# Kernel tuning notes

Measured on AMD Instinct MI355X. Metric: run time of the kernel, lower is better.

The kernel has to match this reference:

```python
import jax, jax.numpy as jnp
import numpy as np

ATOM_DIM = 64
BOND_DIM = 64
B, N_ATOMS, N_BONDS = 32, 256, 512


def setup_inputs() -> dict:
    key = jax.random.key(0)
    k1, k2, k3, k4 = jax.random.split(key, 4)
    atom_state = jax.random.normal(k1, (B, N_ATOMS, ATOM_DIM), dtype=jnp.float32)
    bond_state = jax.random.normal(k2, (B, N_BONDS, BOND_DIM), dtype=jnp.float32)
    connectivity = jax.random.randint(k3, (B, N_BONDS, 2), 0, N_ATOMS, dtype=jnp.int64)
    # glorot-ish scale for the learned bond->matrix projection
    scale = (2.0 / (BOND_DIM + ATOM_DIM * ATOM_DIM)) ** 0.5
    bond_transform = jax.random.normal(k4, (BOND_DIM, ATOM_DIM * ATOM_DIM), dtype=jnp.float32) * scale
    return {
        "atom_state": atom_state,
        "bond_state": bond_state,
        "connectivity": connectivity,
        "bond_transform": bond_transform,
    }


def reference(atom_state, bond_state, connectivity, bond_transform):
    # src atom per edge: gather along atom axis with batch dim (tf.gather batch_dims=1)
    src_idx = connectivity[:, :, 0]                                  # [B, E]
    src_atoms = jnp.take_along_axis(
        atom_state, src_idx[:, :, None], axis=1)                    # [B, E, D]
    # bond embedding -> per-edge DxD matrix
    W = bond_transform.reshape(BOND_DIM, ATOM_DIM, ATOM_DIM)         # [K, D, D]
    bond_weights = jnp.einsum('bek,kij->beij', bond_state, W)        # [B, E, D, D]
    # per-edge matrix-vector message: A_e @ h_src
    messages = jnp.einsum('beij,bej->bei', bond_weights, src_atoms)  # [B, E, D]
    return messages
```

## Files before the change

### kernel.cpp

```cpp
#include <hip/hip_runtime.h>
#include <stdint.h>


#define NATOMS 256
#define DIM 64
#define BM 64

typedef _Float16 f16;
typedef _Float16 f16x2 __attribute__((ext_vector_type(2)));
typedef _Float16 f16x8 __attribute__((ext_vector_type(8)));
typedef float f32x16 __attribute__((ext_vector_type(16)));

#define AS1 __attribute__((address_space(1)))
#define AS3 __attribute__((address_space(3)))

union H8 { f16x8 v8; f16x2 v2[4]; };

static __device__ __forceinline__ void gll16(const void* g, void* l) {
    __builtin_amdgcn_global_load_lds((AS1 void*)(uintptr_t)g, (AS3 void*)l, 16, 0, 0);
}

__global__ __launch_bounds__(256) void prep_w2f(const float* __restrict__ bt,
                                                f16* __restrict__ w2f) {
    const int d  = blockIdx.x * 256 + threadIdx.x;
    const int kg = d >> 9, c = d & 511;
    const int wcq = c >> 8, s = (c >> 6) & 3, l = c & 63;
    const int i = (l & 31) + 32 * wcq;
    const int u = 2 * s + (l >> 5);
    const float* src = bt + (size_t)kg * 4096 + i * 64 + u * 8;
    const float4 p = *reinterpret_cast<const float4*>(src);
    const float4 q = *reinterpret_cast<const float4*>(src + 4);
    const f16x8 h = { (f16)p.x, (f16)p.y, (f16)p.z, (f16)p.w,
                      (f16)q.x, (f16)q.y, (f16)q.z, (f16)q.w };
    reinterpret_cast<f16x8*>(w2f)[d] = h;
}

__global__ __launch_bounds__(256, 1) void bond_msg(
    const float* __restrict__ atom, const float* __restrict__ bond,
    const int* __restrict__ conn, const f16* __restrict__ w2f,
    float* __restrict__ out)
{
    __shared__ __align__(16) unsigned char smem[32768];

    const int tid  = threadIdx.x;
    const int lane = tid & 63;
    const int w    = tid >> 6;
    const int wc   = w & 1;
    const int kh   = w >> 1;
    const int lo   = lane & 31;
    const int hi   = lane >> 5;
    const int blk  = blockIdx.x;
    const int bond0 = blk * BM;

    const int m0 = lo, m1 = lo + 32;
    const int ia0 = conn[(bond0 + m0) * 2];
    const int ia1 = conn[(bond0 + m1) * 2];
    const float* ar0 = atom + (size_t)(blk >> 3) * (NATOMS * DIM) + (size_t)ia0 * DIM;
    const float* ar1 = atom + (size_t)(blk >> 3) * (NATOMS * DIM) + (size_t)ia1 * DIM;
    f16x2 srcv[2][4][4];
    #pragma unroll
    for (int s = 0; s < 4; ++s) {
        const int j0 = s * 16 + hi * 8;
        float4 p0 = *reinterpret_cast<const float4*>(ar0 + j0);
        float4 p1 = *reinterpret_cast<const float4*>(ar0 + j0 + 4);
        float4 q0 = *reinterpret_cast<const float4*>(ar1 + j0);
        float4 q1 = *reinterpret_cast<const float4*>(ar1 + j0 + 4);
        srcv[0][s][0] = (f16x2){ (f16)p0.x, (f16)p0.y };
        srcv[0][s][1] = (f16x2){ (f16)p0.z, (f16)p0.w };
        srcv[0][s][2] = (f16x2){ (f16)p1.x, (f16)p1.y };
        srcv[0][s][3] = (f16x2){ (f16)p1.z, (f16)p1.w };
        srcv[1][s][0] = (f16x2){ (f16)q0.x, (f16)q0.y };
        srcv[1][s][1] = (f16x2){ (f16)q0.z, (f16)q0.w };
        srcv[1][s][2] = (f16x2){ (f16)q1.x, (f16)q1.y };
        srcv[1][s][3] = (f16x2){ (f16)q1.z, (f16)q1.w };
    }

    {
        const char* gb = reinterpret_cast<const char*>(bond + (size_t)bond0 * DIM);
        #pragma unroll
        for (int c = 0; c < 4; ++c)
            gll16(gb + w * 4096 + c * 1024 + lane * 16, smem + w * 4096 + c * 1024);
    }
    __syncthreads();

    {
        const float* bl = reinterpret_cast<const float*>(smem);
        unsigned* btw = reinterpret_cast<unsigned*>(smem + 16384);
        const int k = lane;
        #pragma unroll
        for (int mm = 0; mm < 16; ++mm) {
            const int m = w * 16 + mm;
            const f16 hh = (f16)bl[m * 64 + k];
            const f16x2 d = { hh, hh };
            btw[k * 64 + (m ^ (k & 31))] = __builtin_bit_cast(unsigned, d);
        }
    }
    __syncthreads();

    f32x16 acc0 = {};
    f32x16 acc1 = {};
    const unsigned* btl = reinterpret_cast<const unsigned*>(smem + 16384);
    const char* gw = reinterpret_cast<const char*>(w2f)
                   + (size_t)kh * 32 * 8192 + wc * 4096 + lane * 16;

    f16x8 bufA[4], bufB[4];
    #define LOADIT(buf, it) do {                                          \
        const char* _p = gw + (it) * 8192;                                \
        buf[0] = *reinterpret_cast<const f16x8*>(_p);                     \
        buf[1] = *reinterpret_cast<const f16x8*>(_p + 1024);              \
        buf[2] = *reinterpret_cast<const f16x8*>(_p + 2048);              \
        buf[3] = *reinterpret_cast<const f16x8*>(_p + 3072);              \
    } while (0)

    #define COMPIT(buf, it) do {                                          \
        const int _kg = kh * 32 + (it);                                   \
        const f16x2 _b0 = __builtin_bit_cast(f16x2,                       \
            btl[_kg * 64 + (m0 ^ (_kg & 31))]);                           \
        const f16x2 _b1 = __builtin_bit_cast(f16x2,                       \
            btl[_kg * 64 + (m1 ^ (_kg & 31))]);                           \
        _Pragma("unroll")                                                 \
        for (int s = 0; s < 4; ++s) {                                     \
            H8 _a0, _a1;                                                  \
            _Pragma("unroll")                                             \
            for (int t = 0; t < 4; ++t) {                                 \
                _a0.v2[t] = _b0 * srcv[0][s][t];                          \
                _a1.v2[t] = _b1 * srcv[1][s][t];                          \
            }                                                             \
            acc0 = __builtin_amdgcn_mfma_f32_32x32x16_f16(_a0.v8, buf[s], acc0, 0, 0, 0); \
            acc1 = __builtin_amdgcn_mfma_f32_32x32x16_f16(_a1.v8, buf[s], acc1, 0, 0, 0); \
        }                                                                 \
    } while (0)

    LOADIT(bufA, 0);
    for (int it = 0; it < 32; it += 2) {
        LOADIT(bufB, it + 1);
        COMPIT(bufA, it);
        if (it + 2 < 32) LOADIT(bufA, it + 2);
        COMPIT(bufB, it + 1);
    }

    if (kh == 1) {
        #pragma unroll
        for (int g = 0; g < 4; ++g) {
            float4 v0 = { acc0[4*g+0], acc0[4*g+1], acc0[4*g+2], acc0[4*g+3] };
            *reinterpret_cast<float4*>(smem + wc*8192 + g*1024 + lane*16) = v0;
            float4 v1 = { acc1[4*g+0], acc1[4*g+1], acc1[4*g+2], acc1[4*g+3] };
            *reinterpret_cast<float4*>(smem + wc*8192 + (g+4)*1024 + lane*16) = v1;
        }
    }
    __syncthreads();
    if (kh == 0) {
        #pragma unroll
        for (int g = 0; g < 4; ++g) {
            float4 v0 = *reinterpret_cast<const float4*>(smem + wc*8192 + g*1024 + lane*16);
            acc0[4*g+0] += v0.x; acc0[4*g+1] += v0.y; acc0[4*g+2] += v0.z; acc0[4*g+3] += v0.w;
            float4 v1 = *reinterpret_cast<const float4*>(smem + wc*8192 + (g+4)*1024 + lane*16);
            acc1[4*g+0] += v1.x; acc1[4*g+1] += v1.y; acc1[4*g+2] += v1.z; acc1[4*g+3] += v1.w;
        }
        const int colb = 32 * wc + lo;
        #pragma unroll
        for (int r = 0; r < 16; ++r) {
            const int rl = (r & 3) + 8 * (r >> 2) + 4 * hi;
            out[(size_t)(bond0 + rl) * 64 + colb]      = acc0[r];
            out[(size_t)(bond0 + 32 + rl) * 64 + colb] = acc1[r];
        }
    }
}

__global__ __launch_bounds__(256) void bond_fallback(
    const float* __restrict__ atom, const float* __restrict__ bond,
    const int* __restrict__ conn, const float* __restrict__ bt,
    float* __restrict__ out)
{
    __shared__ float Wk[4096];
    __shared__ float srcs[4][64];
    __shared__ float bnds[4][64];
    const int blk = blockIdx.x;
    const int e0 = blk * 4;
    const int b = e0 >> 9;
    const int t = threadIdx.x;
    const int il = t & 63, eg = t >> 6;
    const int e = e0 + eg;
    const int ia = conn[e * 2];
    srcs[eg][il] = atom[(size_t)b * (NATOMS * DIM) + (size_t)ia * DIM + il];
    bnds[eg][il] = bond[(size_t)e * DIM + il];
    float acc = 0.f;
    for (int k = 0; k < 64; ++k) {
        __syncthreads();
        #pragma unroll
        for (int c = 0; c < 4; ++c) {
            float4 v = reinterpret_cast<const float4*>(bt + (size_t)k * 4096)[t + c * 256];
            reinterpret_cast<float4*>(Wk)[t + c * 256] = v;
        }
        __syncthreads();
        float s = 0.f;
        #pragma unroll
        for (int j = 0; j < 64; ++j) s += Wk[il * 64 + j] * srcs[eg][j];
        acc += bnds[eg][k] * s;
    }
    out[(size_t)e * DIM + il] = acc;
}

extern "C" void kernel_launch(void* const* d_in, const int* in_sizes, int n_in,
                              void* d_out, int out_size, void* d_ws, size_t ws_size,
                              hipStream_t stream) {
    const float* atom = (const float*)d_in[0];
    const float* bond = (const float*)d_in[1];
    const int*   conn = (const int*)d_in[2];
    const float* bt   = (const float*)d_in[3];
    float* out = (float*)d_out;

    if (ws_size >= (size_t)64 * 4096 * sizeof(f16)) {
        f16* w2f = (f16*)d_ws;
        prep_w2f<<<128, 256, 0, stream>>>(bt, w2f);
        bond_msg<<<256, 256, 0, stream>>>(atom, bond, conn, w2f, out);
    } else {
        bond_fallback<<<4096, 256, 0, stream>>>(atom, bond, conn, bt, out);
    }
}
```

Baseline: 24.04 us.

## Stage weight tiles in LDS shared across 8 waves with double-buffered async loads

The bond kernel is restructured so each block handles 128 bonds and one 32-column half of the output, with 8 waves. Four M-tile waves now share weight tiles loaded into LDS via global_load_lds with double buffering, replacing per-wave direct global loads. Per-bond scale factors move into registers instead of a transposed LDS table, and the reduction scratch uses a swizzled layout to avoid bank conflicts. The aim is to cut redundant weight traffic from global memory and overlap loads with MFMA work. The cost is extra barriers per stage and heavier register use from the 32 bond scalars.

```diff
diff --git a/kernel.cpp b/kernel.cpp
--- a/kernel.cpp
+++ b/kernel.cpp
@@ -4,7 +4,7 @@
 
 #define NATOMS 256
 #define DIM 64
-#define BM 64
+#define BT 128
 
 typedef _Float16 f16;
 typedef _Float16 f16x2 __attribute__((ext_vector_type(2)));
@@ -20,14 +20,19 @@
     __builtin_amdgcn_global_load_lds((AS1 void*)(uintptr_t)g, (AS3 void*)l, 16, 0, 0);
 }
 
+static __device__ __forceinline__ void wave_barrier() {
+    __builtin_amdgcn_sched_barrier(0);
+    __builtin_amdgcn_s_barrier();
+    __builtin_amdgcn_sched_barrier(0);
+}
+
 __global__ __launch_bounds__(256) void prep_w2f(const float* __restrict__ bt,
                                                 f16* __restrict__ w2f) {
     const int d  = blockIdx.x * 256 + threadIdx.x;
-    const int kg = d >> 9, c = d & 511;
-    const int wcq = c >> 8, s = (c >> 6) & 3, l = c & 63;
-    const int i = (l & 31) + 32 * wcq;
-    const int u = 2 * s + (l >> 5);
-    const float* src = bt + (size_t)kg * 4096 + i * 64 + u * 8;
+    const int k  = d >> 9, c = d & 511;
+    const int ch = c >> 8, s = (c >> 6) & 3, l = c & 63;
+    const int col = ch * 32 + (l & 31);
+    const float* src = bt + (size_t)k * 4096 + col * 64 + s * 16 + (l >> 5) * 8;
     const float4 p = *reinterpret_cast<const float4*>(src);
     const float4 q = *reinterpret_cast<const float4*>(src + 4);
     const f16x8 h = { (f16)p.x, (f16)p.y, (f16)p.z, (f16)p.w,
@@ -35,134 +40,128 @@
     reinterpret_cast<f16x8*>(w2f)[d] = h;
 }
 
-__global__ __launch_bounds__(256, 1) void bond_msg(
+static __device__ __forceinline__ unsigned swz16(unsigned lane) {
+    return (lane * 16u) ^ ((lane & 0x38u) << 1);
+}
+
+__global__ __launch_bounds__(512, 1) void bond_msg(
     const float* __restrict__ atom, const float* __restrict__ bond,
     const int* __restrict__ conn, const f16* __restrict__ w2f,
     float* __restrict__ out)
 {
-    __shared__ __align__(16) unsigned char smem[32768];
+    __shared__ __align__(16) unsigned char smem[65536];
 
     const int tid  = threadIdx.x;
     const int lane = tid & 63;
     const int w    = tid >> 6;
-    const int wc   = w & 1;
-    const int kh   = w >> 1;
+    const int mt   = w & 3;
+    const int kh   = w >> 2;
     const int lo   = lane & 31;
     const int hi   = lane >> 5;
     const int blk  = blockIdx.x;
-    const int bond0 = blk * BM;
-
-    const int m0 = lo, m1 = lo + 32;
-    const int ia0 = conn[(bond0 + m0) * 2];
-    const int ia1 = conn[(bond0 + m1) * 2];
-    const float* ar0 = atom + (size_t)(blk >> 3) * (NATOMS * DIM) + (size_t)ia0 * DIM;
-    const float* ar1 = atom + (size_t)(blk >> 3) * (NATOMS * DIM) + (size_t)ia1 * DIM;
-    f16x2 srcv[2][4][4];
+    const int btile = blk >> 1;
+    const int ch   = blk & 1;
+    const int bond0 = btile * BT;
+
+    const char* gw = reinterpret_cast<const char*>(w2f)
+                   + (size_t)ch * 4096 + (size_t)lane * 16;
+    char* lst = reinterpret_cast<char*>(smem) + kh * 16384 + mt * 4096;
+    const char* lrd = reinterpret_cast<const char*>(smem) + kh * 16384 + lane * 16;
+
+    #define ISSUE(p) do {                                                 \
+        const char* _g = gw + (size_t)(kh * 32 + (p) * 4 + mt) * 8192;    \
+        char* _l = lst + ((p) & 1) * 32768;                               \
+        gll16(_g,        _l);                                             \
+        gll16(_g + 1024, _l + 1024);                                      \
+        gll16(_g + 2048, _l + 2048);                                      \
+        gll16(_g + 3072, _l + 3072);                                      \
+    } while (0)
+
+    ISSUE(0);
+
+    const int e = bond0 + mt * 32 + lo;
+    const int ia = conn[e * 2];
+    f16x2 bp[32];
+    {
+        const float* brow = bond + (size_t)e * DIM + kh * 32;
+        #pragma unroll
+        for (int q = 0; q < 8; ++q) {
+            const float4 v = *reinterpret_cast<const float4*>(brow + q * 4);
+            const f16 a0 = (f16)v.x, a1 = (f16)v.y, a2 = (f16)v.z, a3 = (f16)v.w;
+            bp[q*4+0] = (f16x2){a0,a0}; bp[q*4+1] = (f16x2){a1,a1};
+            bp[q*4+2] = (f16x2){a2,a2}; bp[q*4+3] = (f16x2){a3,a3};
+        }
+    }
+
+    const float* arow = atom + (size_t)(btile >> 2) * (NATOMS * DIM)
+                      + (size_t)ia * DIM;
+    f16x2 srcv[4][4];
     #pragma unroll
     for (int s = 0; s < 4; ++s) {
         const int j0 = s * 16 + hi * 8;
-        float4 p0 = *reinterpret_cast<const float4*>(ar0 + j0);
-        float4 p1 = *reinterpret_cast<const float4*>(ar0 + j0 + 4);
-        float4 q0 = *reinterpret_cast<const float4*>(ar1 + j0);
-        float4 q1 = *reinterpret_cast<const float4*>(ar1 + j0 + 4);
-        srcv[0][s][0] = (f16x2){ (f16)p0.x, (f16)p0.y };
-        srcv[0][s][1] = (f16x2){ (f16)p0.z, (f16)p0.w };
-        srcv[0][s][2] = (f16x2){ (f16)p1.x, (f16)p1.y };
-        srcv[0][s][3] = (f16x2){ (f16)p1.z, (f16)p1.w };
-        srcv[1][s][0] = (f16x2){ (f16)q0.x, (f16)q0.y };
-        srcv[1][s][1] = (f16x2){ (f16)q0.z, (f16)q0.w };
-        srcv[1][s][2] = (f16x2){ (f16)q1.x, (f16)q1.y };
-        srcv[1][s][3] = (f16x2){ (f16)q1.z, (f16)q1.w };
-    }
-
-    {
-        const char* gb = reinterpret_cast<const char*>(bond + (size_t)bond0 * DIM);
-        #pragma unroll
-        for (int c = 0; c < 4; ++c)
-            gll16(gb + w * 4096 + c * 1024 + lane * 16, smem + w * 4096 + c * 1024);
-    }
+        const float4 p0 = *reinterpret_cast<const float4*>(arow + j0);
+        const float4 p1 = *reinterpret_cast<const float4*>(arow + j0 + 4);
+        srcv[s][0] = (f16x2){ (f16)p0.x, (f16)p0.y };
+        srcv[s][1] = (f16x2){ (f16)p0.z, (f16)p0.w };
+        srcv[s][2] = (f16x2){ (f16)p1.x, (f16)p1.y };
+        srcv[s][3] = (f16x2){ (f16)p1.z, (f16)p1.w };
+    }
+
+    f32x16 acc = {};
+
+    #define STEP(p, wtxt) do {                                            \
+        if ((p) + 1 < 8) ISSUE((p) + 1);                                  \
+        asm volatile("s_waitcnt vmcnt(" wtxt ")" ::: "memory");           \
+        wave_barrier();        \
+        {                                                                 \
+            const char* _rb = lrd + ((p) & 1) * 32768;                    \
+            _Pragma("unroll")                                             \
+            for (int q = 0; q < 4; ++q) {                                 \
+                const f16x2 _c = bp[(p) * 4 + q];                         \
+                _Pragma("unroll")                                         \
+                for (int s = 0; s < 4; ++s) {                             \
+                    const f16x8 bf = *reinterpret_cast<const f16x8*>(     \
+                        _rb + q * 4096 + s * 1024);                       \
+                    H8 _a;                                                \
+                    _Pragma("unroll")                                     \
+                    for (int t = 0; t < 4; ++t) _a.v2[t] = _c * srcv[s][t]; \
+                    acc = __builtin_amdgcn_mfma_f32_32x32x16_f16(_a.v8, bf, acc, 0, 0, 0); \
+                }                                                         \
+            }                                                             \
+        }                                                                 \
+        wave_barrier();                       \
+    } while (0)
+
+    STEP(0, "4"); STEP(1, "4"); STEP(2, "4"); STEP(3, "4");
+    STEP(4, "4"); STEP(5, "4"); STEP(6, "4"); STEP(7, "0");
+
+    #undef STEP
+    #undef ISSUE
+
     __syncthreads();
-
-    {
-        const float* bl = reinterpret_cast<const float*>(smem);
-        unsigned* btw = reinterpret_cast<unsigned*>(smem + 16384);
-        const int k = lane;
-        #pragma unroll
-        for (int mm = 0; mm < 16; ++mm) {
-            const int m = w * 16 + mm;
-            const f16 hh = (f16)bl[m * 64 + k];
-            const f16x2 d = { hh, hh };
-            btw[k * 64 + (m ^ (k & 31))] = __builtin_bit_cast(unsigned, d);
-        }
-    }
-    __syncthreads();
-
-    f32x16 acc0 = {};
-    f32x16 acc1 = {};
-    const unsigned* btl = reinterpret_cast<const unsigned*>(smem + 16384);
-    const char* gw = reinterpret_cast<const char*>(w2f)
-                   + (size_t)kh * 32 * 8192 + wc * 4096 + lane * 16;
-
-    f16x8 bufA[4], bufB[4];
-    #define LOADIT(buf, it) do {                                          \
-        const char* _p = gw + (it) * 8192;                                \
-        buf[0] = *reinterpret_cast<const f16x8*>(_p);                     \
-        buf[1] = *reinterpret_cast<const f16x8*>(_p + 1024);              \
-        buf[2] = *reinterpret_cast<const f16x8*>(_p + 2048);              \
-        buf[3] = *reinterpret_cast<const f16x8*>(_p + 3072);              \
-    } while (0)
-
-    #define COMPIT(buf, it) do {                                          \
-        const int _kg = kh * 32 + (it);                                   \
-        const f16x2 _b0 = __builtin_bit_cast(f16x2,                       \
-            btl[_kg * 64 + (m0 ^ (_kg & 31))]);                           \
-        const f16x2 _b1 = __builtin_bit_cast(f16x2,                       \
-            btl[_kg * 64 + (m1 ^ (_kg & 31))]);                           \
-        _Pragma("unroll")                                                 \
-        for (int s = 0; s < 4; ++s) {                                     \
-            H8 _a0, _a1;                                                  \
-            _Pragma("unroll")                                             \
-            for (int t = 0; t < 4; ++t) {                                 \
-                _a0.v2[t] = _b0 * srcv[0][s][t];                          \
-                _a1.v2[t] = _b1 * srcv[1][s][t];                          \
-            }                                                             \
-            acc0 = __builtin_amdgcn_mfma_f32_32x32x16_f16(_a0.v8, buf[s], acc0, 0, 0, 0); \
-            acc1 = __builtin_amdgcn_mfma_f32_32x32x16_f16(_a1.v8, buf[s], acc1, 0, 0, 0); \
-        }                                                                 \
-    } while (0)
-
-    LOADIT(bufA, 0);
-    for (int it = 0; it < 32; it += 2) {
-        LOADIT(bufB, it + 1);
-        COMPIT(bufA, it);
-        if (it + 2 < 32) LOADIT(bufA, it + 2);
-        COMPIT(bufB, it + 1);
-    }
-
     if (kh == 1) {
+        const unsigned so = swz16((unsigned)lane);
         #pragma unroll
         for (int g = 0; g < 4; ++g) {
-            float4 v0 = { acc0[4*g+0], acc0[4*g+1], acc0[4*g+2], acc0[4*g+3] };
-            *reinterpret_cast<float4*>(smem + wc*8192 + g*1024 + lane*16) = v0;
-            float4 v1 = { acc1[4*g+0], acc1[4*g+1], acc1[4*g+2], acc1[4*g+3] };
-            *reinterpret_cast<float4*>(smem + wc*8192 + (g+4)*1024 + lane*16) = v1;
+            float4 v = { acc[4*g+0], acc[4*g+1], acc[4*g+2], acc[4*g+3] };
+            *reinterpret_cast<float4*>(smem + mt*4096 + g*1024 + so) = v;
         }
     }
     __syncthreads();
     if (kh == 0) {
+        const unsigned so = swz16((unsigned)lane);
         #pragma unroll
         for (int g = 0; g < 4; ++g) {
-            float4 v0 = *reinterpret_cast<const float4*>(smem + wc*8192 + g*1024 + lane*16);
-            acc0[4*g+0] += v0.x; acc0[4*g+1] += v0.y; acc0[4*g+2] += v0.z; acc0[4*g+3] += v0.w;
-            float4 v1 = *reinterpret_cast<const float4*>(smem + wc*8192 + (g+4)*1024 + lane*16);
-            acc1[4*g+0] += v1.x; acc1[4*g+1] += v1.y; acc1[4*g+2] += v1.z; acc1[4*g+3] += v1.w;
-        }
-        const int colb = 32 * wc + lo;
+            const float4 v = *reinterpret_cast<const float4*>(
+                smem + mt*4096 + g*1024 + so);
+            acc[4*g+0] += v.x; acc[4*g+1] += v.y;
+            acc[4*g+2] += v.z; acc[4*g+3] += v.w;
+        }
+        const int colb = ch * 32 + lo;
         #pragma unroll
         for (int r = 0; r < 16; ++r) {
             const int rl = (r & 3) + 8 * (r >> 2) + 4 * hi;
-            out[(size_t)(bond0 + rl) * 64 + colb]      = acc0[r];
-            out[(size_t)(bond0 + 32 + rl) * 64 + colb] = acc1[r];
+            out[(size_t)(bond0 + mt * 32 + rl) * 64 + colb] = acc[r];
         }
     }
 }
@@ -213,7 +212,7 @@
     if (ws_size >= (size_t)64 * 4096 * sizeof(f16)) {
         f16* w2f = (f16*)d_ws;
         prep_w2f<<<128, 256, 0, stream>>>(bt, w2f);
-        bond_msg<<<256, 256, 0, stream>>>(atom, bond, conn, w2f, out);
+        bond_msg<<<256, 512, 0, stream>>>(atom, bond, conn, w2f, out);
     } else {
         bond_fallback<<<4096, 256, 0, stream>>>(atom, bond, conn, bt, out);
     }
```

New measurement: 22.48 us. -6.5%, faster.
